# Kernel tuning notes

Hardware: AMD Instinct MI355X
Metric: run time of the kernel (lower is better)

## Reference

```python
import jax, jax.numpy as jnp
import numpy as np

EPS = 1e-05
N_CLUSTERS = 4


def setup_inputs() -> dict:
    key = jax.random.key(0)
    k1, k2, k3, k4, k5, k6 = jax.random.split(key, 6)
    B, C, H, W = 64, 64, 112, 112
    return {
        "x": jax.random.normal(k1, (B, C, H, W), dtype=jnp.float32),
        "running_mean": jax.random.normal(k2, (C,), dtype=jnp.float32),
        "running_var": jax.random.uniform(k3, (C,), dtype=jnp.float32),
        "weight": jax.random.normal(k4, (C,), dtype=jnp.float32),
        "bias": jax.random.normal(k5, (C,), dtype=jnp.float32),
        "labels": jax.random.randint(k6, (B,), 0, N_CLUSTERS, dtype=jnp.int32),
    }


def reference(x, running_mean, running_var, weight, bias, labels):
    B, C, H, W = x.shape
    hw = H * W
    # per-sample partial sums over spatial dims -> [B, C]
    s = jnp.sum(x, axis=(2, 3))
    ss = jnp.sum(x * x, axis=(2, 3))
    # per-cluster reductions over the batch (gather-reduce) -> [G, C]
    S = jax.ops.segment_sum(s, labels, num_segments=N_CLUSTERS)
    SS = jax.ops.segment_sum(ss, labels, num_segments=N_CLUSTERS)
    cnt = jax.ops.segment_sum(jnp.ones((B,), x.dtype), labels, num_segments=N_CLUSTERS)
    N = cnt[:, None] * hw  # elements per (cluster, channel)
    mean_g = S / jnp.maximum(N, 1.0)
    # unbiased variance (ddof=1), matching torch.var_mean(unbiased=True)
    var_g = (SS - N * mean_g * mean_g) / jnp.maximum(N - 1.0, 1.0)
    # blended stats: 0.2 * cluster + 0.8 * running (BN source) stats; scatter back per sample
    mu = 0.2 * mean_g[labels] + 0.8 * running_mean[None, :]      # [B, C]
    var = 0.2 * var_g[labels] + 0.8 * running_var[None, :]       # [B, C]
    x_n = (x - mu[:, :, None, None]) * jax.lax.rsqrt(var + EPS)[:, :, None, None]
    return x_n * weight[None, :, None, None] + bias[None, :, None, None]
```

## Files before the change

### kernel.cpp

```cpp
#include <hip/hip_runtime.h>

#define HW    12544
#define HW4   3136
#define NCH   64
#define NB    64
#define EPSF  1e-5f

typedef float fvec4 __attribute__((ext_vector_type(4)));


__global__ __launch_bounds__(256) void cn_stats(const float* __restrict__ x,
                                                float* __restrict__ ws) {
    int p = blockIdx.x;
    const fvec4* xp = (const fvec4*)(x + (size_t)p * HW);
    float s = 0.0f, ss = 0.0f;
    for (int i = threadIdx.x; i < HW4; i += 256) {
        fvec4 v = xp[i];
        s  += v.x + v.y + v.z + v.w;
        ss += v.x * v.x + v.y * v.y + v.z * v.z + v.w * v.w;
    }
    #pragma unroll
    for (int off = 32; off > 0; off >>= 1) {
        s  += __shfl_down(s, off, 64);
        ss += __shfl_down(ss, off, 64);
    }
    __shared__ float sh[8];
    int lane = threadIdx.x & 63;
    int wave = threadIdx.x >> 6;
    if (lane == 0) { sh[wave] = s; sh[4 + wave] = ss; }
    __syncthreads();
    if (threadIdx.x == 0) {
        ws[p]        = sh[0] + sh[1] + sh[2] + sh[3];
        ws[4096 + p] = sh[4] + sh[5] + sh[6] + sh[7];
    }
}

__global__ __launch_bounds__(256) void cn_norm(const float* __restrict__ x,
                                               const int* __restrict__ labels,
                                               const float* __restrict__ rmean,
                                               const float* __restrict__ rvar,
                                               const float* __restrict__ wgt,
                                               const float* __restrict__ bia,
                                               const float* __restrict__ ws,
                                               float* __restrict__ out) {
    int p = blockIdx.x;
    int b = p >> 6;
    int c = p & 63;
    __shared__ float sh_scale, sh_shift;
    if (threadIdx.x < 64) {
        int t = threadIdx.x;
        int g  = labels[b];
        int lb = labels[t];
        bool m = (lb == g);
        float s   = m ? ws[t * NCH + c]        : 0.0f;
        float ss  = m ? ws[4096 + t * NCH + c] : 0.0f;
        float cnt = m ? 1.0f : 0.0f;
        #pragma unroll
        for (int off = 32; off > 0; off >>= 1) {
            s   += __shfl_down(s,   off, 64);
            ss  += __shfl_down(ss,  off, 64);
            cnt += __shfl_down(cnt, off, 64);
        }
        if (t == 0) {
            float N    = cnt * (float)HW;
            float mean = s / fmaxf(N, 1.0f);
            float var  = (ss - N * mean * mean) / fmaxf(N - 1.0f, 1.0f);
            float mu   = 0.2f * mean + 0.8f * rmean[c];
            float vb   = 0.2f * var  + 0.8f * rvar[c];
            float scale = rsqrtf(vb + EPSF) * wgt[c];
            sh_scale = scale;
            sh_shift = bia[c] - mu * scale;
        }
    }
    __syncthreads();
    float scale = sh_scale;
    float shift = sh_shift;
    const fvec4* xp = (const fvec4*)(x + (size_t)p * HW);
    fvec4*       op = (fvec4*)(out + (size_t)p * HW);
    for (int i = threadIdx.x; i < HW4; i += 256) {
        fvec4 v = xp[i];
        fvec4 o;
        o.x = v.x * scale + shift;
        o.y = v.y * scale + shift;
        o.z = v.z * scale + shift;
        o.w = v.w * scale + shift;
        __builtin_nontemporal_store(o, &op[i]);
    }
}

extern "C" void kernel_launch(void* const* d_in, const int* in_sizes, int n_in,
                              void* d_out, int out_size, void* d_ws, size_t ws_size,
                              hipStream_t stream) {
    const float* x      = (const float*)d_in[0];
    const float* rmean  = (const float*)d_in[1];
    const float* rvar   = (const float*)d_in[2];
    const float* wgt    = (const float*)d_in[3];
    const float* bia    = (const float*)d_in[4];
    const int*   labels = (const int*)d_in[5];
    float* out = (float*)d_out;
    float* ws  = (float*)d_ws;

    const int planes = NB * NCH;

    cn_stats<<<planes, 256, 0, stream>>>(x, ws);
    cn_norm<<<planes, 256, 0, stream>>>(x, labels, rmean, rvar, wgt, bia, ws, out);
}
```

Baseline: 96.71 us.

## Split stats/normalize into two channel halves for cache reuse

Splits the stats and normalize passes into two rounds, each over half of the channels (about 100 MB of input per half). The aim is that the second read of x in the normalize kernel hits the large last-level cache instead of HBM. Normalize loads are also marked nontemporal, since the data is not reused after that point. The trade-off is twice as many kernel launches, smaller grids per launch, and dependence on the cache being large enough to hold a half.

```diff
diff --git a/kernel.cpp b/kernel.cpp
--- a/kernel.cpp
+++ b/kernel.cpp
@@ -9,9 +9,12 @@
 typedef float fvec4 __attribute__((ext_vector_type(4)));
 
 
-__global__ __launch_bounds__(256) void cn_stats(const float* __restrict__ x,
-                                                float* __restrict__ ws) {
-    int p = blockIdx.x;
+__global__ __launch_bounds__(256) void cn_stats_half(const float* __restrict__ x,
+                                                     float* __restrict__ ws,
+                                                     int c0) {
+    int c = (blockIdx.x & 31) + c0;
+    int b = blockIdx.x >> 5;
+    int p = b * NCH + c;
     const fvec4* xp = (const fvec4*)(x + (size_t)p * HW);
     float s = 0.0f, ss = 0.0f;
     for (int i = threadIdx.x; i < HW4; i += 256) {
@@ -35,17 +38,18 @@
     }
 }
 
-__global__ __launch_bounds__(256) void cn_norm(const float* __restrict__ x,
-                                               const int* __restrict__ labels,
-                                               const float* __restrict__ rmean,
-                                               const float* __restrict__ rvar,
-                                               const float* __restrict__ wgt,
-                                               const float* __restrict__ bia,
-                                               const float* __restrict__ ws,
-                                               float* __restrict__ out) {
-    int p = blockIdx.x;
-    int b = p >> 6;
-    int c = p & 63;
+__global__ __launch_bounds__(256) void cn_norm_half(const float* __restrict__ x,
+                                                    const int* __restrict__ labels,
+                                                    const float* __restrict__ rmean,
+                                                    const float* __restrict__ rvar,
+                                                    const float* __restrict__ wgt,
+                                                    const float* __restrict__ bia,
+                                                    const float* __restrict__ ws,
+                                                    float* __restrict__ out,
+                                                    int c0) {
+    int c = (blockIdx.x & 31) + c0;
+    int b = blockIdx.x >> 5;
+    int p = b * NCH + c;
     __shared__ float sh_scale, sh_shift;
     if (threadIdx.x < 64) {
         int t = threadIdx.x;
@@ -78,7 +82,7 @@
     const fvec4* xp = (const fvec4*)(x + (size_t)p * HW);
     fvec4*       op = (fvec4*)(out + (size_t)p * HW);
     for (int i = threadIdx.x; i < HW4; i += 256) {
-        fvec4 v = xp[i];
+        fvec4 v = __builtin_nontemporal_load(&xp[i]);
         fvec4 o;
         o.x = v.x * scale + shift;
         o.y = v.y * scale + shift;
@@ -100,8 +104,10 @@
     float* out = (float*)d_out;
     float* ws  = (float*)d_ws;
 
-    const int planes = NB * NCH;
+    const int half = NB * (NCH / 2);
 
-    cn_stats<<<planes, 256, 0, stream>>>(x, ws);
-    cn_norm<<<planes, 256, 0, stream>>>(x, labels, rmean, rvar, wgt, bia, ws, out);
+    cn_stats_half<<<half, 256, 0, stream>>>(x, ws, 0);
+    cn_norm_half <<<half, 256, 0, stream>>>(x, labels, rmean, rvar, wgt, bia, ws, out, 0);
+    cn_stats_half<<<half, 256, 0, stream>>>(x, ws, 32);
+    cn_norm_half <<<half, 256, 0, stream>>>(x, labels, rmean, rvar, wgt, bia, ws, out, 32);
 }
```

New measurement: 101.2 us. +4.7%, slower.

## Fuse stats and normalize into cooperative kernel caching planes in registers and LDS

Applied to the files above, without the earlier changes.

Replaces the two-kernel stats/normalize pass with a single cooperative grid kernel of 1024 blocks. Each wave owns one plane: it computes the sums, keeps 16 of its 49 float4 chunks in registers and 8 in LDS, then crosses a grid-wide barrier and normalizes. This saves roughly half of the second read of x from HBM and one kernel launch. The cost is a grid sync, heavy register and LDS use that must still allow all 1024 blocks to be co-resident, and a fallback to the old path if the cooperative launch fails.

```diff
diff --git a/kernel.cpp b/kernel.cpp
--- a/kernel.cpp
+++ b/kernel.cpp
@@ -1,12 +1,108 @@
 #include <hip/hip_runtime.h>
+#include <hip/hip_cooperative_groups.h>
+
+namespace cg = cooperative_groups;
 
 #define HW    12544
 #define HW4   3136
 #define NCH   64
-#define NB    64
 #define EPSF  1e-5f
 
 typedef float fvec4 __attribute__((ext_vector_type(4)));
+
+#define RREG  16
+#define RLDS  8
+#define RTOT  49
+
+
+__global__ __launch_bounds__(256, 4) void cn_fused(
+    const float* __restrict__ x, const int* __restrict__ labels,
+    const float* __restrict__ rmean, const float* __restrict__ rvar,
+    const float* __restrict__ wgt, const float* __restrict__ bia,
+    float* __restrict__ ws, float* __restrict__ out)
+{
+    __shared__ fvec4 lds4[4 * RLDS * 64];
+
+    const int l = threadIdx.x & 63;
+    const int w = threadIdx.x >> 6;
+    const int p = blockIdx.x * 4 + w;
+    const int b = p >> 6;
+    const int c = p & 63;
+
+    const fvec4* xp = (const fvec4*)(x + (size_t)p * HW);
+    fvec4* lw = lds4 + w * (RLDS * 64);
+
+    fvec4 r[RREG];
+    float s = 0.0f, ss = 0.0f;
+    #pragma unroll
+    for (int k = 0; k < RREG; ++k) {
+        fvec4 v = xp[k * 64 + l];
+        r[k] = v;
+        s  += v.x + v.y + v.z + v.w;
+        ss += v.x * v.x + v.y * v.y + v.z * v.z + v.w * v.w;
+    }
+    #pragma unroll
+    for (int k = RREG; k < RREG + RLDS; ++k) {
+        fvec4 v = xp[k * 64 + l];
+        lw[(k - RREG) * 64 + l] = v;
+        s  += v.x + v.y + v.z + v.w;
+        ss += v.x * v.x + v.y * v.y + v.z * v.z + v.w * v.w;
+    }
+    #pragma unroll
+    for (int k = RREG + RLDS; k < RTOT; ++k) {
+        fvec4 v = xp[k * 64 + l];
+        s  += v.x + v.y + v.z + v.w;
+        ss += v.x * v.x + v.y * v.y + v.z * v.z + v.w * v.w;
+    }
+    #pragma unroll
+    for (int off = 32; off > 0; off >>= 1) {
+        s  += __shfl_xor(s,  off, 64);
+        ss += __shfl_xor(ss, off, 64);
+    }
+    if (l == 0) { ws[p] = s; ws[4096 + p] = ss; }
+
+    __threadfence();
+    cg::this_grid().sync();
+
+    int g  = labels[b];
+    int lb = labels[l];
+    bool m = (lb == g);
+    float s2  = m ? ws[l * NCH + c]        : 0.0f;
+    float ss2 = m ? ws[4096 + l * NCH + c] : 0.0f;
+    float cnt = m ? 1.0f : 0.0f;
+    #pragma unroll
+    for (int off = 32; off > 0; off >>= 1) {
+        s2  += __shfl_xor(s2,  off, 64);
+        ss2 += __shfl_xor(ss2, off, 64);
+        cnt += __shfl_xor(cnt, off, 64);
+    }
+    float N    = cnt * (float)HW;
+    float mean = s2 / fmaxf(N, 1.0f);
+    float var  = (ss2 - N * mean * mean) / fmaxf(N - 1.0f, 1.0f);
+    float mu   = 0.2f * mean + 0.8f * rmean[c];
+    float vb   = 0.2f * var  + 0.8f * rvar[c];
+    float scale = rsqrtf(vb + EPSF) * wgt[c];
+    float shift = bia[c] - mu * scale;
+
+    fvec4* op = (fvec4*)(out + (size_t)p * HW);
+    #pragma unroll
+    for (int k = 0; k < RREG; ++k) {
+        fvec4 o = r[k] * scale + shift;
+        __builtin_nontemporal_store(o, &op[k * 64 + l]);
+    }
+    #pragma unroll
+    for (int k = RREG; k < RREG + RLDS; ++k) {
+        fvec4 v = lw[(k - RREG) * 64 + l];
+        fvec4 o = v * scale + shift;
+        __builtin_nontemporal_store(o, &op[k * 64 + l]);
+    }
+    #pragma unroll
+    for (int k = RREG + RLDS; k < RTOT; ++k) {
+        fvec4 v = xp[k * 64 + l];
+        fvec4 o = v * scale + shift;
+        __builtin_nontemporal_store(o, &op[k * 64 + l]);
+    }
+}
 
 
 __global__ __launch_bounds__(256) void cn_stats(const float* __restrict__ x,
@@ -48,7 +144,7 @@
     int c = p & 63;
     __shared__ float sh_scale, sh_shift;
     if (threadIdx.x < 64) {
-        int t = threadIdx.x;
+        int t  = threadIdx.x;
         int g  = labels[b];
         int lb = labels[t];
         bool m = (lb == g);
@@ -100,8 +196,13 @@
     float* out = (float*)d_out;
     float* ws  = (float*)d_ws;
 
-    const int planes = NB * NCH;
-
-    cn_stats<<<planes, 256, 0, stream>>>(x, ws);
-    cn_norm<<<planes, 256, 0, stream>>>(x, labels, rmean, rvar, wgt, bia, ws, out);
-}
+    void* args[] = {(void*)&x, (void*)&labels, (void*)&rmean, (void*)&rvar,
+                    (void*)&wgt, (void*)&bia, (void*)&ws, (void*)&out};
+    hipError_t err = hipLaunchCooperativeKernel((const void*)cn_fused, dim3(1024),
+                                                dim3(256), args, 0, stream);
+    if (err != hipSuccess) {
+        const int planes = 64 * NCH;
+        cn_stats<<<planes, 256, 0, stream>>>(x, ws);
+        cn_norm <<<planes, 256, 0, stream>>>(x, labels, rmean, rvar, wgt, bia, ws, out);
+    }
+}
```

Result: slower. 367.7 us (+280.2%).
